# Kernel optimization log

Hardware: AMD Instinct MI355X
Metric: run time of the kernel (lower is better)

The kernel has to match this reference:

```python
import jax, jax.numpy as jnp
import numpy as np

HEAD_SIZE = 12
INNER_DIM = 64
BIG_NEG = 1e12


def _sinusoidal(seq_len, dim):
    # interleaved [sin, cos, sin, cos, ...] like SinusoidalPositionEmbedding('zero')
    pos = jnp.arange(seq_len, dtype=jnp.float32)
    inv = jnp.power(10000.0, -2.0 * jnp.arange(dim // 2, dtype=jnp.float32) / dim)
    ang = pos[:, None] * inv[None, :]                       # (L, dim/2)
    return jnp.stack([jnp.sin(ang), jnp.cos(ang)], axis=-1).reshape(seq_len, dim)


def _rope_rotate(x, cos_pos, sin_pos):
    # x: (B, L, H, D); rotate-half per interleaved RoPE
    x2 = jnp.stack([-x[..., 1::2], x[..., ::2]], axis=-1).reshape(x.shape)
    return x * cos_pos + x2 * sin_pos


def setup_inputs() -> dict:
    key = jax.random.key(0)
    k1, k2 = jax.random.split(key)
    B, L, HID = 16, 512, 768
    sequence_output = jax.random.normal(k1, (B, L, HID), dtype=jnp.float32)
    mask = jnp.ones((B, L), dtype=jnp.float32)
    W = jax.random.normal(k2, (HID, HEAD_SIZE * INNER_DIM * 2), dtype=jnp.float32) * 0.02
    b = jnp.zeros((HEAD_SIZE * INNER_DIM * 2,), dtype=jnp.float32)
    return {"sequence_output": sequence_output, "mask": mask, "W": W, "b": b}


def reference(sequence_output, mask, W, b):
    B, L, _ = sequence_output.shape
    H, D = HEAD_SIZE, INNER_DIM
    out = sequence_output @ W + b                           # (B, L, H*2D)
    out = out.reshape(B, L, H, 2 * D)
    qw, kw = out[..., :D], out[..., D:]                     # (B, L, H, D)
    pos = _sinusoidal(L, D)                                 # (L, D)
    cos_pos = jnp.repeat(pos[:, None, 1::2], 2, axis=-1)    # (L, 1, D)
    sin_pos = jnp.repeat(pos[:, None, ::2], 2, axis=-1)
    qw = _rope_rotate(qw, cos_pos, sin_pos)
    kw = _rope_rotate(kw, cos_pos, sin_pos)
    logits = jnp.einsum('bmhd,bnhd->bhmn', qw, kw)          # (B, H, L, L)
    pad = mask[:, None, None, :]                            # (B, 1, 1, L)
    logits = logits * pad - (1.0 - pad) * BIG_NEG
    tril = jnp.tril(jnp.ones((L, L), dtype=logits.dtype), -1)
    logits = logits - tril * BIG_NEG
    return logits / (D ** 0.5)
```

## Files before the change

### kernel.cpp

```cpp
#include <hip/hip_runtime.h>
#include <stdint.h>

typedef float f32x4 __attribute__((ext_vector_type(4)));
typedef unsigned long long u64;

#define HEADS 12
#define DDIM 64
#define LSEQ 512
#define HID 768
#define NOUT 1536
#define BIG_NEG 1000000000000.0f

__device__ __forceinline__ void gl_lds16(const void* g, void* l) {
    __builtin_amdgcn_global_load_lds(
        (const __attribute__((address_space(1))) void*)g,
        (__attribute__((address_space(3))) void*)l, 16, 0, 0);
}

__device__ __forceinline__ void ldsbar() {
    asm volatile("s_waitcnt lgkmcnt(0)" ::: "memory");
    __builtin_amdgcn_s_barrier();
}

__device__ __forceinline__ uint32_t pk4_fp8(float a, float b, float c, float d) {
    uint32_t v = __builtin_amdgcn_cvt_pk_fp8_f32(a, b, 0, false);
    v = __builtin_amdgcn_cvt_pk_fp8_f32(c, d, v, true);
    return v;
}

__global__ __launch_bounds__(256) void prep_k(
    const float* __restrict__ X, const float* __restrict__ W,
    uint8_t* __restrict__ Xq, uint8_t* __restrict__ Wtq,
    float* __restrict__ cosT, float* __restrict__ sinT) {

    int blk = blockIdx.x;
    if (blk < 3072) {
        size_t idx = ((size_t)blk * 256 + threadIdx.x) * 8;
        float4 f0 = *(const float4*)(X + idx);
        float4 f1 = *(const float4*)(X + idx + 4);
        uint2 p;
        p.x = pk4_fp8(f0.x, f0.y, f0.z, f0.w);
        p.y = pk4_fp8(f1.x, f1.y, f1.z, f1.w);
        *(uint2*)(Xq + idx) = p;
    } else if (blk < 4224) {
        __shared__ float Ls[32][33];
        int b2 = blk - 3072;
        int n0 = (b2 % 48) * 32, k0 = (b2 / 48) * 32;
        int tx = threadIdx.x & 31, ty = threadIdx.x >> 5;
#pragma unroll
        for (int rr = 0; rr < 4; ++rr) {
            int k = ty + rr * 8;
            Ls[k][tx] = W[(size_t)(k0 + k) * NOUT + n0 + tx];
        }
        __syncthreads();
        int n = threadIdx.x >> 3, c = threadIdx.x & 7;
        uint32_t w = pk4_fp8(Ls[4*c][n], Ls[4*c+1][n], Ls[4*c+2][n], Ls[4*c+3][n]);
        *(uint32_t*)(Wtq + (size_t)(n0 + n) * HID + k0 + c * 4) = w;
    } else {
        int idx = (blk - 4224) * 256 + threadIdx.x;
        int l = idx >> 6, d = idx & 63;
        int p = d >> 1;
        float inv = powf(10000.0f, (-2.0f * (float)p) / 64.0f);
        float ang = (float)l * inv;
        cosT[idx] = cosf(ang);
        sinT[idx] = sinf(ang);
    }
}

__global__ __launch_bounds__(256) void proj_rope_k(
    const uint8_t* __restrict__ Xq, const uint8_t* __restrict__ Wtq,
    const float* __restrict__ bias, const float* __restrict__ cosT,
    const float* __restrict__ sinT,
    uint8_t* __restrict__ qq, uint8_t* __restrict__ kq) {

    __shared__ __align__(16) uint8_t As[128 * 64];
    __shared__ __align__(16) uint8_t Bs[128 * 64];

    const int tid = threadIdx.x;
    const int m0 = blockIdx.x * 128, n0 = blockIdx.y * 128;
    const int lane = tid & 63, wid = tid >> 6;
    const int wm = wid >> 1, wn = wid & 1;
    const int lr = lane & 15, kg = lane >> 4;

    const int srow = tid >> 2, sc = tid & 3;

    f32x4 acc[4][4] = {};

    for (int k0 = 0; k0 < HID; k0 += 64) {
#pragma unroll
        for (int j = 0; j < 2; ++j) {
            int r = j * 64 + srow;
            int cs = sc ^ ((r >> 1) & 3);
            gl_lds16(Wtq + (size_t)(n0 + r) * HID + k0 + cs * 16,
                     Bs + j * 4096 + tid * 16);
            gl_lds16(Xq + (size_t)(m0 + r) * HID + k0 + cs * 16,
                     As + j * 4096 + tid * 16);
        }
        __syncthreads();
#pragma unroll
        for (int ks = 0; ks < 2; ++ks) {
            u64 af[4], xf[4];
#pragma unroll
            for (int ai = 0; ai < 4; ++ai) {
                int row = wn * 64 + ai * 16 + lr;
                int sl = (ks * 4 + kg) ^ (row & 6);
                af[ai] = *(const u64*)(Bs + row * 64 + sl * 8);
            }
#pragma unroll
            for (int bi = 0; bi < 4; ++bi) {
                int row = wm * 64 + bi * 16 + lr;
                int sl = (ks * 4 + kg) ^ (row & 6);
                xf[bi] = *(const u64*)(As + row * 64 + sl * 8);
            }
#pragma unroll
            for (int ai = 0; ai < 4; ++ai)
#pragma unroll
                for (int bi = 0; bi < 4; ++bi)
                    acc[ai][bi] = __builtin_amdgcn_mfma_f32_16x16x32_fp8_fp8(
                        (long long)af[ai], (long long)xf[bi], acc[ai][bi], 0, 0, 0);
        }
        __syncthreads();
    }

#pragma unroll
    for (int ai = 0; ai < 4; ++ai) {
        int nb = n0 + wn * 64 + ai * 16 + kg * 4;
        int h = nb >> 7, d2 = nb & 127;
        int d = d2 & 63;
        uint8_t* dst = (d2 >= 64) ? kq : qq;
        float4 b4 = *(const float4*)&bias[nb];
#pragma unroll
        for (int bi = 0; bi < 4; ++bi) {
            int m = m0 + wm * 64 + bi * 16 + lr;
            int bidx = m >> 9, lpos = m & 511;
            float4 c4 = *(const float4*)&cosT[lpos * 64 + d];
            float4 s4 = *(const float4*)&sinT[lpos * 64 + d];
            float v0 = acc[ai][bi][0] + b4.x;
            float v1 = acc[ai][bi][1] + b4.y;
            float v2 = acc[ai][bi][2] + b4.z;
            float v3 = acc[ai][bi][3] + b4.w;
            float o0 = v0 * c4.x - v1 * s4.x;
            float o1 = v1 * c4.y + v0 * s4.y;
            float o2 = v2 * c4.z - v3 * s4.z;
            float o3 = v3 * c4.w + v2 * s4.w;
            uint32_t pw = pk4_fp8(o0, o1, o2, o3);
            *(uint32_t*)(dst + (((size_t)bidx * HEADS + h) * LSEQ + lpos) * DDIM + d) = pw;
        }
    }
}

__global__ __launch_bounds__(256) void attn_k(
    const uint8_t* __restrict__ qq, const uint8_t* __restrict__ kq,
    const float* __restrict__ mask, float* __restrict__ out) {

    __shared__ __align__(16) uint8_t Qs[8192];
    __shared__ __align__(16) uint8_t Ks[8192];
    __shared__ __align__(16) float Es[32 * 132];
    __shared__ int wok[4];

    const int tid = threadIdx.x;
    const int bid = blockIdx.x;
    const int L = (bid & 7) * 96 + (bid >> 3);
    const int bh = L >> 2;
    const int mtile = L & 3;
    const int m0 = mtile * 128;
    const int lane = tid & 63, wid = tid >> 6;
    const int wm = wid >> 1, wn = wid & 1;
    const int lr = lane & 15, kg = lane >> 4;
    const int b = bh / HEADS;

    int myok = 1;
    for (int c0 = tid; c0 < m0; c0 += 256)
        myok &= (mask[b * LSEQ + c0] == 1.0f) ? 1 : 0;
    unsigned long long bal = __ballot(myok);
    if (lane == 0) wok[wid] = (bal == ~0ull) ? 1 : 0;
    ldsbar();
    const int nstart = (wok[0] & wok[1] & wok[2] & wok[3]) ? mtile : 0;

    const uint8_t* qbase = qq + ((size_t)bh * LSEQ + m0) * DDIM;
    const uint8_t* kbase = kq + (size_t)bh * LSEQ * DDIM;

    const int srow = tid >> 2, sc = tid & 3;
#pragma unroll
    for (int j = 0; j < 2; ++j) {
        int r = j * 64 + srow;
        int cs = sc ^ ((r >> 1) & 3);
        gl_lds16(qbase + (size_t)r * DDIM + cs * 16, Qs + j * 4096 + tid * 16);
        gl_lds16(kbase + (size_t)(nstart * 128 + r) * DDIM + cs * 16,
                 Ks + j * 4096 + tid * 16);
    }
    __syncthreads();

    const int colb = (tid & 31) * 4;
    const int rrow = tid >> 5;
    float* obase = out + (size_t)bh * LSEQ * LSEQ;

    for (int nt = nstart; nt < 4; ++nt) {
        f32x4 acc[4][4] = {};
#pragma unroll
        for (int ks = 0; ks < 2; ++ks) {
            u64 af[4], qf[4];
#pragma unroll
            for (int ai = 0; ai < 4; ++ai) {
                int row = wn * 64 + ai * 16 + lr;
                int sl = (ks * 4 + kg) ^ (row & 6);
                af[ai] = *(const u64*)(Ks + row * 64 + sl * 8);
            }
#pragma unroll
            for (int bi = 0; bi < 4; ++bi) {
                int row = wm * 64 + bi * 16 + lr;
                int sl = (ks * 4 + kg) ^ (row & 6);
                qf[bi] = *(const u64*)(Qs + row * 64 + sl * 8);
            }
#pragma unroll
            for (int ai = 0; ai < 4; ++ai)
#pragma unroll
                for (int bi = 0; bi < 4; ++bi)
                    acc[ai][bi] = __builtin_amdgcn_mfma_f32_16x16x32_fp8_fp8(
                        (long long)af[ai], (long long)qf[bi], acc[ai][bi], 0, 0, 0);
        }
        ldsbar();

        const int n0 = nt * 128;
        const float4 p4 = *(const float4*)&mask[b * LSEQ + n0 + colb];

        if (nt < 3) {
#pragma unroll
            for (int j = 0; j < 2; ++j) {
                int r = j * 64 + srow;
                int cs = sc ^ ((r >> 1) & 3);
                gl_lds16(kbase + (size_t)((nt + 1) * 128 + r) * DDIM + cs * 16,
                         Ks + j * 4096 + tid * 16);
            }
        }

#pragma unroll
        for (int p = 0; p < 4; ++p) {
            ldsbar();
            if (wm == (p >> 1)) {
                const int bi0 = (p & 1) * 2;
#pragma unroll
                for (int bb = 0; bb < 2; ++bb) {
                    int bi = bi0 + bb;
                    int row = bb * 16 + lr;
#pragma unroll
                    for (int ai = 0; ai < 4; ++ai) {
                        int n = wn * 64 + ai * 16 + kg * 4;
                        *(f32x4*)&Es[row * 132 + n] = acc[ai][bi];
                    }
                }
            }
            ldsbar();
#pragma unroll
            for (int j = 0; j < 4; ++j) {
                int rloc = rrow + j * 8;
                int m = m0 + p * 32 + rloc;
                f32x4 v = *(f32x4*)&Es[rloc * 132 + colb];
                int n = n0 + colb;
                f32x4 o;
                o[0] = (v[0] * p4.x - (1.0f - p4.x) * BIG_NEG
                        - ((m > n + 0) ? BIG_NEG : 0.0f)) * 0.125f;
                o[1] = (v[1] * p4.y - (1.0f - p4.y) * BIG_NEG
                        - ((m > n + 1) ? BIG_NEG : 0.0f)) * 0.125f;
                o[2] = (v[2] * p4.z - (1.0f - p4.z) * BIG_NEG
                        - ((m > n + 2) ? BIG_NEG : 0.0f)) * 0.125f;
                o[3] = (v[3] * p4.w - (1.0f - p4.w) * BIG_NEG
                        - ((m > n + 3) ? BIG_NEG : 0.0f)) * 0.125f;
                __builtin_nontemporal_store(o, (f32x4*)&obase[(size_t)m * LSEQ + n]);
            }
        }

        if (nt < 3) {
            asm volatile("s_waitcnt vmcnt(16) lgkmcnt(0)" ::: "memory");
            __builtin_amdgcn_s_barrier();
        }
    }

    const float CONSTV = (-BIG_NEG) * 0.125f;
    f32x4 cv = {CONSTV, CONSTV, CONSTV, CONSTV};
    for (int nt2 = 0; nt2 < nstart; ++nt2) {
        int n = nt2 * 128 + colb;
#pragma unroll
        for (int p = 0; p < 4; ++p)
#pragma unroll
            for (int j = 0; j < 4; ++j) {
                int m = m0 + p * 32 + rrow + j * 8;
                __builtin_nontemporal_store(cv, (f32x4*)&obase[(size_t)m * LSEQ + n]);
            }
    }
}

extern "C" void kernel_launch(void* const* d_in, const int* in_sizes, int n_in,
                              void* d_out, int out_size, void* d_ws, size_t ws_size,
                              hipStream_t stream) {
    const float* X    = (const float*)d_in[0];
    const float* mask = (const float*)d_in[1];
    const float* W    = (const float*)d_in[2];
    const float* bias = (const float*)d_in[3];
    float* out = (float*)d_out;

    char* ws = (char*)d_ws;
    float*   cosT = (float*)ws;
    float*   sinT = (float*)(ws + 131072);
    uint8_t* Wtq  = (uint8_t*)(ws + 262144);
    uint8_t* Xq   = (uint8_t*)(ws + 1441792);
    uint8_t* qq   = (uint8_t*)(ws + 7733248);
    uint8_t* kq   = (uint8_t*)(ws + 14024704);

    prep_k<<<4352, 256, 0, stream>>>(X, W, Xq, Wtq, cosT, sinT);
    proj_rope_k<<<dim3(64, 12), 256, 0, stream>>>(Xq, Wtq, bias, cosT, sinT, qq, kq);
    attn_k<<<768, 256, 0, stream>>>(qq, kq, mask, out);
}
```

Before: 83.54 us.

## Double-buffer LDS tiles in fp8 projection GEMM to overlap loads with MFMA

Splits the shared-memory A/B tiles into two buffers and issues the global-to-LDS loads for the next K-slice before computing on the current one. Explicit vmcnt waits and barriers replace the two __syncthreads per iteration. The aim is to hide global memory latency behind MFMA work in the projection kernel. LDS use doubles to 32KB per block, which may lower occupancy, and correctness depends on the hand-written waitcnt counts.

```diff
diff --git a/kernel.cpp b/kernel.cpp
--- a/kernel.cpp
+++ b/kernel.cpp
@@ -73,8 +73,8 @@
     const float* __restrict__ sinT,
     uint8_t* __restrict__ qq, uint8_t* __restrict__ kq) {
 
-    __shared__ __align__(16) uint8_t As[128 * 64];
-    __shared__ __align__(16) uint8_t Bs[128 * 64];
+    __shared__ __align__(16) uint8_t As[2][128 * 64];
+    __shared__ __align__(16) uint8_t Bs[2][128 * 64];
 
     const int tid = threadIdx.x;
     const int m0 = blockIdx.x * 128, n0 = blockIdx.y * 128;
@@ -86,17 +86,33 @@
 
     f32x4 acc[4][4] = {};
 
-    for (int k0 = 0; k0 < HID; k0 += 64) {
-#pragma unroll
-        for (int j = 0; j < 2; ++j) {
-            int r = j * 64 + srow;
-            int cs = sc ^ ((r >> 1) & 3);
-            gl_lds16(Wtq + (size_t)(n0 + r) * HID + k0 + cs * 16,
-                     Bs + j * 4096 + tid * 16);
-            gl_lds16(Xq + (size_t)(m0 + r) * HID + k0 + cs * 16,
-                     As + j * 4096 + tid * 16);
-        }
-        __syncthreads();
+#pragma unroll
+    for (int j = 0; j < 2; ++j) {
+        int r = j * 64 + srow;
+        int cs = sc ^ ((r >> 1) & 3);
+        gl_lds16(Wtq + (size_t)(n0 + r) * HID + cs * 16, Bs[0] + j * 4096 + tid * 16);
+        gl_lds16(Xq  + (size_t)(m0 + r) * HID + cs * 16, As[0] + j * 4096 + tid * 16);
+    }
+
+    for (int it = 0; it < 12; ++it) {
+        const int cur = it & 1;
+        if (it < 11) {
+            const int k0 = (it + 1) * 64;
+#pragma unroll
+            for (int j = 0; j < 2; ++j) {
+                int r = j * 64 + srow;
+                int cs = sc ^ ((r >> 1) & 3);
+                gl_lds16(Wtq + (size_t)(n0 + r) * HID + k0 + cs * 16,
+                         Bs[cur ^ 1] + j * 4096 + tid * 16);
+                gl_lds16(Xq  + (size_t)(m0 + r) * HID + k0 + cs * 16,
+                         As[cur ^ 1] + j * 4096 + tid * 16);
+            }
+            asm volatile("s_waitcnt vmcnt(4)" ::: "memory");
+        } else {
+            asm volatile("s_waitcnt vmcnt(0)" ::: "memory");
+        }
+        __builtin_amdgcn_s_barrier();
+
 #pragma unroll
         for (int ks = 0; ks < 2; ++ks) {
             u64 af[4], xf[4];
@@ -104,13 +120,13 @@
             for (int ai = 0; ai < 4; ++ai) {
                 int row = wn * 64 + ai * 16 + lr;
                 int sl = (ks * 4 + kg) ^ (row & 6);
-                af[ai] = *(const u64*)(Bs + row * 64 + sl * 8);
+                af[ai] = *(const u64*)(Bs[cur] + row * 64 + sl * 8);
             }
 #pragma unroll
             for (int bi = 0; bi < 4; ++bi) {
                 int row = wm * 64 + bi * 16 + lr;
                 int sl = (ks * 4 + kg) ^ (row & 6);
-                xf[bi] = *(const u64*)(As + row * 64 + sl * 8);
+                xf[bi] = *(const u64*)(As[cur] + row * 64 + sl * 8);
             }
 #pragma unroll
             for (int ai = 0; ai < 4; ++ai)
@@ -119,7 +135,7 @@
                     acc[ai][bi] = __builtin_amdgcn_mfma_f32_16x16x32_fp8_fp8(
                         (long long)af[ai], (long long)xf[bi], acc[ai][bi], 0, 0, 0);
         }
-        __syncthreads();
+        ldsbar();
     }
 
 #pragma unroll
```

Result: faster. 77.25 us (-7.5%).
